# Kernel optimization log

Measured on AMD Instinct MI355X. Metric: run time of the kernel, lower is better.

The kernel has to match this reference:

```python
import jax, jax.numpy as jnp
import numpy as np

# --- HashGrid constants (from init_kwargs) ---
L = 16                 # num_lods
T = 1 << 18            # hashmap entries per level (codebook_bitwidth=18)
F = 2                  # feature_dim per level
BASE = 16              # min_width_codebook
MAXW = 1 << 12         # max_width_codebook
SCALE = np.exp((np.log(MAXW) - np.log(BASE)) / L)
RES = np.floor(BASE * SCALE ** np.arange(L)).astype(np.float32)  # per-level grid resolution
P1 = np.uint32(2654435761)  # coherent-prime hash primes (prime for x is 1)
P2 = np.uint32(805459861)
OFFS = np.array([[i, j, k] for i in (0, 1) for j in (0, 1) for k in (0, 1)], np.int32)  # [8,3] cube corners


def _hash_encode(x, tables):
    """x: [N,3] in [0,1]. tables: [L,T,F]. Returns [N, 3 + L*F] (include_xyz)."""
    def level(table, res):
        xs = x * res                              # [N,3] scaled coords
        x0 = jnp.floor(xs)
        t = xs - x0                               # fractional part
        w = t * t * (3.0 - 2.0 * t)               # Smoothstep interpolation weights
        c = x0.astype(jnp.int32)[:, None, :] + OFFS[None]    # [N,8,3] corner coords
        cu = c.astype(jnp.uint32)
        h = (cu[..., 0] ^ (cu[..., 1] * P1) ^ (cu[..., 2] * P2)) & jnp.uint32(T - 1)  # [N,8]
        feats = table[h]                          # [N,8,F] irregular gather
        wts = jnp.prod(jnp.where(OFFS[None] == 1, w[:, None, :], 1.0 - w[:, None, :]), axis=-1)  # [N,8]
        return jnp.einsum('ncf,nc->nf', feats, wts)  # [N,F]

    f = jax.vmap(level)(tables, jnp.asarray(RES))   # [L,N,F]
    f = jnp.moveaxis(f, 0, 1).reshape(x.shape[0], L * F)
    return jnp.concatenate([x, f], axis=-1)         # include_xyz prepends raw coords


def setup_inputs() -> dict:
    key = jax.random.key(0)
    k1, k2, k3, k4 = jax.random.split(key, 4)
    N = 1 << 20
    x = jax.random.uniform(k1, (N, 3), dtype=jnp.float32)
    tables = jax.random.normal(k2, (L, T, F), dtype=jnp.float32) * 1e-2
    d_in = 3 + L * F    # 35
    W1 = jax.random.normal(k3, (d_in, 128), dtype=jnp.float32) / np.sqrt(d_in)
    W2 = jax.random.normal(k4, (128, 129), dtype=jnp.float32) / np.sqrt(128.0)
    return {"x": x, "tables": tables, "W1": W1, "W2": W2}


def reference(x, tables, W1, W2):
    enc = _hash_encode(x, tables)        # [N,35]
    h = jax.nn.relu(enc @ W1)            # VanillaMLP: one hidden layer, bias-free
    return h @ W2                        # [N, 1+geo_feat_dim], Identity output act
```

## Files before the change

kernel.cpp:

```cpp
#include <hip/hip_runtime.h>

typedef __attribute__((ext_vector_type(8))) short short8;
typedef __attribute__((ext_vector_type(4))) short short4v;
typedef __attribute__((ext_vector_type(4))) float f32x4;

#define TMASK  ((1u << 18) - 1u)
#define PRIME1 2654435761u
#define PRIME2 805459861u

__constant__ float c_res[16] = {16.f, 22.f, 31.f, 45.f, 63.f, 90.f, 127.f, 181.f,
                                255.f, 362.f, 511.f, 724.f, 1023.f, 1448.f, 2047.f, 2896.f};

__device__ __forceinline__ unsigned short rne_bf16(float v) {
  unsigned u = __builtin_bit_cast(unsigned, v);
  return (unsigned short)((u + 0x7fffu + ((u >> 16) & 1u)) >> 16);
}
__device__ __forceinline__ float b2f(unsigned short h) {
  unsigned u = (unsigned)h << 16;
  return __builtin_bit_cast(float, u);
}

__global__ __launch_bounds__(256) void encode_lvl(
    const float* __restrict__ X, const float* __restrict__ Tb,
    unsigned short* __restrict__ encF) {
  const int b = blockIdx.x;
  const int g = b & 7;
  const int p = (b >> 3) * 256 + threadIdx.x;

  const float x0 = X[p * 3 + 0];
  const float x1 = X[p * 3 + 1];
  const float x2 = X[p * 3 + 2];

  short4v pk;
#pragma unroll
  for (int li = 0; li < 2; ++li) {
    const int lvl = 2 * g + li;
    const float r = c_res[lvl];
    const float xs0 = x0 * r, xs1 = x1 * r, xs2 = x2 * r;
    const float f0 = floorf(xs0), f1 = floorf(xs1), f2 = floorf(xs2);
    const float t0 = xs0 - f0, t1 = xs1 - f1, t2 = xs2 - f2;
    const float w0 = t0 * t0 * (3.f - 2.f * t0);
    const float w1v = t1 * t1 * (3.f - 2.f * t1);
    const float w2v = t2 * t2 * (3.f - 2.f * t2);
    const unsigned cx0 = (unsigned)(int)f0;
    const unsigned hy0 = (unsigned)(int)f1 * PRIME1, hy1 = hy0 + PRIME1;
    const unsigned hz0 = (unsigned)(int)f2 * PRIME2, hz1 = hz0 + PRIME2;
    const float2* tab = reinterpret_cast<const float2*>(Tb) + ((size_t)lvl << 18);
    float a0 = 0.f, a1 = 0.f;
    if (!(cx0 & 1u)) {
      const float4* tab4 = reinterpret_cast<const float4*>(tab);
#pragma unroll
      for (int jk = 0; jk < 4; ++jk) {
        const unsigned hb = (cx0 ^ ((jk & 2) ? hy1 : hy0) ^ ((jk & 1) ? hz1 : hz0)) & TMASK;
        const float4 q = tab4[hb >> 1];
        float e0x, e0y, e1x, e1y;
        if (hb & 1) { e0x = q.z; e0y = q.w; e1x = q.x; e1y = q.y; }
        else        { e0x = q.x; e0y = q.y; e1x = q.z; e1y = q.w; }
        const float wy = (jk & 2) ? w1v : 1.f - w1v;
        const float wz = (jk & 1) ? w2v : 1.f - w2v;
        const float wt0 = ((1.f - w0) * wy) * wz;
        const float wt1 = (w0 * wy) * wz;
        a0 = fmaf(e0x, wt0, a0);
        a1 = fmaf(e0y, wt0, a1);
        a0 = fmaf(e1x, wt1, a0);
        a1 = fmaf(e1y, wt1, a1);
      }
    } else {
#pragma unroll
      for (int c = 0; c < 8; ++c) {
        const unsigned hx = cx0 + (unsigned)((c >> 2) & 1);
        const unsigned hh = (hx ^ ((c & 2) ? hy1 : hy0) ^ ((c & 1) ? hz1 : hz0)) & TMASK;
        const float2 f = tab[hh];
        const float wt = (((c >> 2) & 1) ? w0 : 1.f - w0) *
                         (((c >> 1) & 1) ? w1v : 1.f - w1v) *
                         (((c & 1)) ? w2v : 1.f - w2v);
        a0 = fmaf(f.x, wt, a0);
        a1 = fmaf(f.y, wt, a1);
      }
    }
    pk[li * 2 + 0] = (short)rne_bf16(a0);
    pk[li * 2 + 1] = (short)rne_bf16(a1);
  }
  const int pl = p & 63, chunk = p >> 6;
  const size_t addr = ((size_t)(chunk * 4 + (pl >> 4)) * 64 +
                       (((g >> 1) << 4) | (pl & 15))) * 8 + (g & 1) * 4;
  *reinterpret_cast<short4v*>(encF + addr) = pk;
}

__global__ __launch_bounds__(256, 2) void mlp_mfma(
    const float* __restrict__ X, const float* __restrict__ W1,
    const float* __restrict__ W2, const unsigned short* __restrict__ encF,
    float* __restrict__ Out, int nChunks) {
  __shared__ __align__(16) unsigned char lds[76800];
  unsigned short* w1S  = (unsigned short*)lds;
  float*          w1x  = (float*)(lds + 8192);
  float*          xyzS = (float*)(lds + 9728);
  unsigned short* w2hS = (unsigned short*)(lds + 10752);
  float*          hS   = (float*)(lds + 43776);
  float*          outS = (float*)(lds + 43776);

  const int tid = threadIdx.x;
  const int lane = tid & 63, w = tid >> 6;

  for (int idx = tid; idx < 32 * 128; idx += 256) {
    const int k = idx >> 7, col = idx & 127;
    w1S[((k >> 3) * 128 + col) * 8 + (k & 7)] = rne_bf16(W1[(k + 3) * 128 + col]);
  }
  for (int idx = tid; idx < 3 * 128; idx += 256) w1x[idx] = W1[idx];
  for (int idx = tid; idx < 128 * 129; idx += 256) {
    const int k = idx / 129, col = idx - k * 129;
    w2hS[((k >> 3) * 129 + col) * 8 + (k & 7)] = rne_bf16(W2[idx]);
  }
  __syncthreads();

  const int stride = gridDim.x;
  int chunk = blockIdx.x;

  short8 af;
  float xv = 0.f;
  if (chunk < nChunks) {
    af = *reinterpret_cast<const short8*>(encF + ((size_t)(chunk * 4 + w) * 64 + lane) * 8);
    if (tid < 192) xv = X[(size_t)(chunk << 6) * 3 + tid];
  }

  for (; chunk < nChunks; chunk += stride) {
    const int row0 = chunk << 6;
    if (tid < 192) xyzS[(tid / 3) * 4 + (tid % 3)] = xv;
    __syncthreads();

    f32x4 acc1[8];
#pragma unroll
    for (int c = 0; c < 8; ++c) acc1[c] = (f32x4){0.f, 0.f, 0.f, 0.f};
#pragma unroll
    for (int c = 0; c < 8; ++c) {
      const short8 b = *reinterpret_cast<const short8*>(
          &w1S[((lane >> 4) * 128 + c * 16 + (lane & 15)) * 8]);
      acc1[c] = __builtin_amdgcn_mfma_f32_16x16x32_bf16(af, b, acc1[c], 0, 0, 0);
    }

    const int nxt = chunk + stride;
    short8 afn;
    if (nxt < nChunks) {
      afn = *reinterpret_cast<const short8*>(encF + ((size_t)(nxt * 4 + w) * 64 + lane) * 8);
      if (tid < 192) xv = X[(size_t)(nxt << 6) * 3 + tid];
    }

#pragma unroll
    for (int r = 0; r < 4; ++r) {
      const int grow = (w << 4) + (lane >> 4) * 4 + r;
      const float xs0 = xyzS[grow * 4 + 0];
      const float xs1 = xyzS[grow * 4 + 1];
      const float xs2 = xyzS[grow * 4 + 2];
#pragma unroll
      for (int c = 0; c < 8; ++c) {
        const int col = c * 16 + (lane & 15);
        float v = acc1[c][r];
        v = fmaf(xs0, w1x[col], v);
        v = fmaf(xs1, w1x[128 + col], v);
        v = fmaf(xs2, w1x[256 + col], v);
        acc1[c][r] = v;
      }
    }
#pragma unroll
    for (int c = 0; c < 8; ++c) {
#pragma unroll
      for (int r = 0; r < 4; ++r) {
        const int row = (w << 4) + (lane >> 4) * 4 + r;
        const int col = c * 16 + (lane & 15);
        const int cc = (col >> 2) ^ (row & 7);
        hS[row * 128 + (cc << 2) + (col & 3)] = fmaxf(acc1[c][r], 0.f);
      }
    }
    __syncthreads();

    {
      const int arow = (w << 4) + (lane & 15);
      short8 a2h[4], a2l[4];
#pragma unroll
      for (int kc = 0; kc < 4; ++kc) {
        const int c8 = kc * 4 + (lane >> 4);
        const int base = arow * 128;
        const int cc0 = (2 * c8) ^ (arow & 7);
        const int cc1 = (2 * c8 + 1) ^ (arow & 7);
        const f32x4 q0 = *reinterpret_cast<const f32x4*>(&hS[base + (cc0 << 2)]);
        const f32x4 q1 = *reinterpret_cast<const f32x4*>(&hS[base + (cc1 << 2)]);
#pragma unroll
        for (int e = 0; e < 4; ++e) {
          const unsigned short hi = rne_bf16(q0[e]);
          a2h[kc][e] = (short)hi;
          a2l[kc][e] = (short)rne_bf16(q0[e] - b2f(hi));
        }
#pragma unroll
        for (int e = 0; e < 4; ++e) {
          const unsigned short hi = rne_bf16(q1[e]);
          a2h[kc][4 + e] = (short)hi;
          a2l[kc][4 + e] = (short)rne_bf16(q1[e] - b2f(hi));
        }
      }
      __syncthreads();

#pragma unroll
      for (int c = 0; c < 9; ++c) {
        f32x4 acc = (f32x4){0.f, 0.f, 0.f, 0.f};
        int bcol = c * 16 + (lane & 15);
        if (bcol > 128) bcol = 128;
#pragma unroll
        for (int kc = 0; kc < 4; ++kc) {
          const int c8 = kc * 4 + (lane >> 4);
          const short8 bh = *reinterpret_cast<const short8*>(&w2hS[(c8 * 129 + bcol) * 8]);
          acc = __builtin_amdgcn_mfma_f32_16x16x32_bf16(a2h[kc], bh, acc, 0, 0, 0);
          acc = __builtin_amdgcn_mfma_f32_16x16x32_bf16(a2l[kc], bh, acc, 0, 0, 0);
        }
        const int col = c * 16 + (lane & 15);
        if (col < 129) {
#pragma unroll
          for (int r = 0; r < 4; ++r) {
            const int lrow = (w << 4) + (lane >> 4) * 4 + r;
            outS[lrow * 129 + col] = acc[r];
          }
        }
      }
    }
    __syncthreads();

    {
      float* dst = Out + (size_t)row0 * 129;
      const f32x4* src = (const f32x4*)outS;
      for (int i = tid; i < 2064; i += 256)
        *reinterpret_cast<f32x4*>(dst + 4 * i) = src[i];
    }
    af = afn;
  }
}

__global__ __launch_bounds__(256) void fused_hashmlp(
    const float* __restrict__ X, const float* __restrict__ Tb,
    const float* __restrict__ W1, const float* __restrict__ W2,
    float* __restrict__ Out, int nChunks) {
  __shared__ __align__(16) unsigned char lds[147968];
  unsigned short* w1hS = (unsigned short*)lds;
  unsigned short* w1lS = w1hS + 128 * 64;
  unsigned short* w2hS = (unsigned short*)(lds + 32768);
  unsigned short* w2lS = w2hS + 129 * 128;
  unsigned short* enchS = (unsigned short*)(lds + 98816);
  unsigned short* enclS = enchS + 64 * 64;
  float*          hS    = (float*)(lds + 115200);
  float*          outS  = (float*)(lds + 98816);

  const int tid = threadIdx.x;
  for (int idx = tid; idx < 128 * 64; idx += 256) {
    int k = idx >> 7, col = idx & 127;
    float v = 0.f;
    if (k < 35) { int r = (k < 32) ? (k + 3) : (k - 32); v = W1[r * 128 + col]; }
    unsigned short hi = rne_bf16(v);
    unsigned short lo = rne_bf16(v - b2f(hi));
    int a = col * 64 + (k ^ ((col & 7) << 3));
    w1hS[a] = hi; w1lS[a] = lo;
  }
  for (int idx = tid; idx < 129 * 128; idx += 256) {
    int k = idx / 129, col = idx - k * 129;
    float v = W2[k * 129 + col];
    unsigned short hi = rne_bf16(v);
    unsigned short lo = rne_bf16(v - b2f(hi));
    int a = col * 128 + (k ^ ((col & 7) << 3));
    w2hS[a] = hi; w2lS[a] = lo;
  }
  __syncthreads();

  const int p = tid >> 2, s = tid & 3, lane = tid & 63, w = tid >> 6;
  for (int chunk = blockIdx.x; chunk < nChunks; chunk += gridDim.x) {
    const int row0 = chunk * 64;
    {
      const int gp = row0 + p;
      const float x0 = X[gp * 3 + 0], x1 = X[gp * 3 + 1], x2 = X[gp * 3 + 2];
      short8 pkh, pkl;
#pragma unroll
      for (int li = 0; li < 4; ++li) {
        const int lvl = (s << 2) + li;
        const float r = c_res[lvl];
        const float xs0 = x0 * r, xs1 = x1 * r, xs2 = x2 * r;
        const float f0 = floorf(xs0), f1 = floorf(xs1), f2 = floorf(xs2);
        const float t0 = xs0 - f0, t1 = xs1 - f1, t2 = xs2 - f2;
        const float w0 = t0 * t0 * (3.f - 2.f * t0);
        const float w1v = t1 * t1 * (3.f - 2.f * t1);
        const float w2v = t2 * t2 * (3.f - 2.f * t2);
        const unsigned cx0 = (unsigned)(int)f0;
        const unsigned hy0 = (unsigned)(int)f1 * PRIME1, hy1 = hy0 + PRIME1;
        const unsigned hz0 = (unsigned)(int)f2 * PRIME2, hz1 = hz0 + PRIME2;
        const float2* tab = reinterpret_cast<const float2*>(Tb) + ((size_t)lvl << 18);
        float a0 = 0.f, a1 = 0.f;
#pragma unroll
        for (int c = 0; c < 8; ++c) {
          const unsigned hx = cx0 + (unsigned)((c >> 2) & 1);
          const unsigned hh = (hx ^ ((c & 2) ? hy1 : hy0) ^ ((c & 1) ? hz1 : hz0)) & TMASK;
          const float2 f = tab[hh];
          const float wt = (((c >> 2) & 1) ? w0 : 1.f - w0) *
                           (((c >> 1) & 1) ? w1v : 1.f - w1v) *
                           (((c & 1)) ? w2v : 1.f - w2v);
          a0 = fmaf(f.x, wt, a0);
          a1 = fmaf(f.y, wt, a1);
        }
        unsigned short h0 = rne_bf16(a0), h1 = rne_bf16(a1);
        pkh[li * 2 + 0] = (short)h0; pkh[li * 2 + 1] = (short)h1;
        pkl[li * 2 + 0] = (short)rne_bf16(a0 - b2f(h0));
        pkl[li * 2 + 1] = (short)rne_bf16(a1 - b2f(h1));
      }
      const int coff = (s ^ (p & 7)) << 3;
      *reinterpret_cast<short8*>(&enchS[p * 64 + coff]) = pkh;
      *reinterpret_cast<short8*>(&enclS[p * 64 + coff]) = pkl;
      short8 zh, zl;
#pragma unroll
      for (int e = 0; e < 8; ++e) { zh[e] = 0; zl[e] = 0; }
      if (s == 0) {
        unsigned short hx0 = rne_bf16(x0), hx1 = rne_bf16(x1), hx2 = rne_bf16(x2);
        zh[0] = (short)hx0; zh[1] = (short)hx1; zh[2] = (short)hx2;
        zl[0] = (short)rne_bf16(x0 - b2f(hx0));
        zl[1] = (short)rne_bf16(x1 - b2f(hx1));
        zl[2] = (short)rne_bf16(x2 - b2f(hx2));
      }
      const int coff2 = ((4 + s) ^ (p & 7)) << 3;
      *reinterpret_cast<short8*>(&enchS[p * 64 + coff2]) = zh;
      *reinterpret_cast<short8*>(&enclS[p * 64 + coff2]) = zl;
    }
    __syncthreads();
    f32x4 acc1[8];
#pragma unroll
    for (int c = 0; c < 8; ++c) acc1[c] = (f32x4){0.f, 0.f, 0.f, 0.f};
    {
      const int arow = (w << 4) + (lane & 15);
#pragma unroll
      for (int kc = 0; kc < 2; ++kc) {
        const int c8 = kc * 4 + (lane >> 4);
        const int aoff = arow * 64 + ((c8 ^ (arow & 7)) << 3);
        const short8 ah = *reinterpret_cast<const short8*>(&enchS[aoff]);
        const short8 al = *reinterpret_cast<const short8*>(&enclS[aoff]);
#pragma unroll
        for (int c = 0; c < 8; ++c) {
          const int bcol = c * 16 + (lane & 15);
          const int boff = bcol * 64 + ((c8 ^ (bcol & 7)) << 3);
          const short8 bh = *reinterpret_cast<const short8*>(&w1hS[boff]);
          const short8 bl = *reinterpret_cast<const short8*>(&w1lS[boff]);
          acc1[c] = __builtin_amdgcn_mfma_f32_16x16x32_bf16(ah, bh, acc1[c], 0, 0, 0);
          acc1[c] = __builtin_amdgcn_mfma_f32_16x16x32_bf16(ah, bl, acc1[c], 0, 0, 0);
          acc1[c] = __builtin_amdgcn_mfma_f32_16x16x32_bf16(al, bh, acc1[c], 0, 0, 0);
        }
      }
    }
#pragma unroll
    for (int c = 0; c < 8; ++c) {
#pragma unroll
      for (int r = 0; r < 4; ++r) {
        const int row = (w << 4) + (lane >> 4) * 4 + r;
        const int col = c * 16 + (lane & 15);
        const int cc = (col >> 2) ^ (row & 7);
        hS[row * 128 + (cc << 2) + (col & 3)] = fmaxf(acc1[c][r], 0.f);
      }
    }
    __syncthreads();
    {
      const int arow = (w << 4) + (lane & 15);
      short8 a2h[4], a2l[4];
#pragma unroll
      for (int kc = 0; kc < 4; ++kc) {
        const int c8 = kc * 4 + (lane >> 4);
        const int base = arow * 128;
        const int cc0 = (2 * c8) ^ (arow & 7);
        const int cc1 = (2 * c8 + 1) ^ (arow & 7);
        const f32x4 q0 = *reinterpret_cast<const f32x4*>(&hS[base + (cc0 << 2)]);
        const f32x4 q1 = *reinterpret_cast<const f32x4*>(&hS[base + (cc1 << 2)]);
#pragma unroll
        for (int e = 0; e < 4; ++e) {
          unsigned short hi = rne_bf16(q0[e]);
          a2h[kc][e] = (short)hi;
          a2l[kc][e] = (short)rne_bf16(q0[e] - b2f(hi));
        }
#pragma unroll
        for (int e = 0; e < 4; ++e) {
          unsigned short hi = rne_bf16(q1[e]);
          a2h[kc][4 + e] = (short)hi;
          a2l[kc][4 + e] = (short)rne_bf16(q1[e] - b2f(hi));
        }
      }
      __syncthreads();
#pragma unroll
      for (int c = 0; c < 9; ++c) {
        f32x4 acc = (f32x4){0.f, 0.f, 0.f, 0.f};
        int bcol = c * 16 + (lane & 15);
        if (bcol > 128) bcol = 128;
#pragma unroll
        for (int kc = 0; kc < 4; ++kc) {
          const int c8 = kc * 4 + (lane >> 4);
          const int boff = bcol * 128 + ((c8 ^ (bcol & 7)) << 3);
          const short8 bh = *reinterpret_cast<const short8*>(&w2hS[boff]);
          const short8 bl = *reinterpret_cast<const short8*>(&w2lS[boff]);
          acc = __builtin_amdgcn_mfma_f32_16x16x32_bf16(a2h[kc], bh, acc, 0, 0, 0);
          acc = __builtin_amdgcn_mfma_f32_16x16x32_bf16(a2h[kc], bl, acc, 0, 0, 0);
          acc = __builtin_amdgcn_mfma_f32_16x16x32_bf16(a2l[kc], bh, acc, 0, 0, 0);
        }
        const int col = c * 16 + (lane & 15);
        if (col < 129) {
#pragma unroll
          for (int r = 0; r < 4; ++r) {
            const int lrow = (w << 4) + (lane >> 4) * 4 + r;
            outS[lrow * 129 + col] = acc[r];
          }
        }
      }
    }
    __syncthreads();
    {
      float* dst = Out + (size_t)row0 * 129;
      const f32x4* src = (const f32x4*)outS;
      for (int i = tid; i < 2064; i += 256)
        *reinterpret_cast<f32x4*>(dst + 4 * i) = src[i];
    }
    __syncthreads();
  }
}

extern "C" void kernel_launch(void* const* d_in, const int* in_sizes, int n_in,
                              void* d_out, int out_size, void* d_ws, size_t ws_size,
                              hipStream_t stream) {
  const float* X  = (const float*)d_in[0];
  const float* Tb = (const float*)d_in[1];
  const float* W1 = (const float*)d_in[2];
  const float* W2 = (const float*)d_in[3];
  float* Out = (float*)d_out;

  const int N = in_sizes[0] / 3;
  const int nChunks = N / 64;

  const size_t encBytes = (size_t)nChunks * 4096;
  if (ws_size >= encBytes && (N & 255) == 0) {
    unsigned short* encF = (unsigned short*)d_ws;
    encode_lvl<<<(N / 256) * 8, 256, 0, stream>>>(X, Tb, encF);
    mlp_mfma<<<2048, 256, 0, stream>>>(X, W1, W2, encF, Out, nChunks);
  } else {
    int grid = nChunks < 1024 ? nChunks : 1024;
    fused_hashmlp<<<grid, 256, 0, stream>>>(X, Tb, W1, W2, Out, nChunks);
  }
}
```

Measured before the change: 577.9 us.

## Fuse encode and MLP into one persistent kernel with flag-based producer-consumer sync

Replaces the separate encode and MLP kernels with one persistent kernel of 512 blocks. Each block encodes a level pair (g, 15-g) for groups of 256 points and signals completion through per-group atomic counters. Blocks then run the MFMA MLP on chunks whose counters reach 8, spinning with s_sleep when none are ready. This overlaps gather-bound encoding with compute-bound MLP work and removes the second launch. The cost is atomics, system-scope loads, a memset, and a specialization to N = 2^20. The design also depends on all 512 blocks being co-resident to avoid deadlock, and it drops the prefetch of the next chunk.

```diff
diff --git a/kernel.cpp b/kernel.cpp
--- a/kernel.cpp
+++ b/kernel.cpp
@@ -1,8 +1,8 @@
 #include <hip/hip_runtime.h>
 
 typedef __attribute__((ext_vector_type(8))) short short8;
-typedef __attribute__((ext_vector_type(4))) short short4v;
 typedef __attribute__((ext_vector_type(4))) float f32x4;
+typedef __attribute__((ext_vector_type(4))) int int4v;
 
 #define TMASK  ((1u << 18) - 1u)
 #define PRIME1 2654435761u
@@ -20,78 +20,59 @@
   return __builtin_bit_cast(float, u);
 }
 
-__global__ __launch_bounds__(256) void encode_lvl(
+__device__ __forceinline__ float2 enc_level(float x0, float x1, float x2, int lvl,
+                                            const float* __restrict__ Tb) {
+  const float r = c_res[lvl];
+  const float xs0 = x0 * r, xs1 = x1 * r, xs2 = x2 * r;
+  const float f0 = floorf(xs0), f1 = floorf(xs1), f2 = floorf(xs2);
+  const float t0 = xs0 - f0, t1 = xs1 - f1, t2 = xs2 - f2;
+  const float w0 = t0 * t0 * (3.f - 2.f * t0);
+  const float w1v = t1 * t1 * (3.f - 2.f * t1);
+  const float w2v = t2 * t2 * (3.f - 2.f * t2);
+  const unsigned cx0 = (unsigned)(int)f0;
+  const unsigned hy0 = (unsigned)(int)f1 * PRIME1, hy1 = hy0 + PRIME1;
+  const unsigned hz0 = (unsigned)(int)f2 * PRIME2, hz1 = hz0 + PRIME2;
+  const float2* tab = reinterpret_cast<const float2*>(Tb) + ((size_t)lvl << 18);
+  float a0 = 0.f, a1 = 0.f;
+  if (!(cx0 & 1u)) {
+    const float4* tab4 = reinterpret_cast<const float4*>(tab);
+#pragma unroll
+    for (int jk = 0; jk < 4; ++jk) {
+      const unsigned hb = (cx0 ^ ((jk & 2) ? hy1 : hy0) ^ ((jk & 1) ? hz1 : hz0)) & TMASK;
+      const float4 q = tab4[hb >> 1];
+      float e0x, e0y, e1x, e1y;
+      if (hb & 1) { e0x = q.z; e0y = q.w; e1x = q.x; e1y = q.y; }
+      else        { e0x = q.x; e0y = q.y; e1x = q.z; e1y = q.w; }
+      const float wy = (jk & 2) ? w1v : 1.f - w1v;
+      const float wz = (jk & 1) ? w2v : 1.f - w2v;
+      const float wt0 = ((1.f - w0) * wy) * wz;
+      const float wt1 = (w0 * wy) * wz;
+      a0 = fmaf(e0x, wt0, a0); a1 = fmaf(e0y, wt0, a1);
+      a0 = fmaf(e1x, wt1, a0); a1 = fmaf(e1y, wt1, a1);
+    }
+  } else {
+#pragma unroll
+    for (int c = 0; c < 8; ++c) {
+      const unsigned hx = cx0 + (unsigned)((c >> 2) & 1);
+      const unsigned hh = (hx ^ ((c & 2) ? hy1 : hy0) ^ ((c & 1) ? hz1 : hz0)) & TMASK;
+      const float2 f = tab[hh];
+      const float wt = (((c >> 2) & 1) ? w0 : 1.f - w0) *
+                       (((c >> 1) & 1) ? w1v : 1.f - w1v) *
+                       (((c & 1)) ? w2v : 1.f - w2v);
+      a0 = fmaf(f.x, wt, a0);
+      a1 = fmaf(f.y, wt, a1);
+    }
+  }
+  return make_float2(a0, a1);
+}
+
+__global__ __launch_bounds__(256, 2) void fused_pc(
     const float* __restrict__ X, const float* __restrict__ Tb,
-    unsigned short* __restrict__ encF) {
-  const int b = blockIdx.x;
-  const int g = b & 7;
-  const int p = (b >> 3) * 256 + threadIdx.x;
-
-  const float x0 = X[p * 3 + 0];
-  const float x1 = X[p * 3 + 1];
-  const float x2 = X[p * 3 + 2];
-
-  short4v pk;
-#pragma unroll
-  for (int li = 0; li < 2; ++li) {
-    const int lvl = 2 * g + li;
-    const float r = c_res[lvl];
-    const float xs0 = x0 * r, xs1 = x1 * r, xs2 = x2 * r;
-    const float f0 = floorf(xs0), f1 = floorf(xs1), f2 = floorf(xs2);
-    const float t0 = xs0 - f0, t1 = xs1 - f1, t2 = xs2 - f2;
-    const float w0 = t0 * t0 * (3.f - 2.f * t0);
-    const float w1v = t1 * t1 * (3.f - 2.f * t1);
-    const float w2v = t2 * t2 * (3.f - 2.f * t2);
-    const unsigned cx0 = (unsigned)(int)f0;
-    const unsigned hy0 = (unsigned)(int)f1 * PRIME1, hy1 = hy0 + PRIME1;
-    const unsigned hz0 = (unsigned)(int)f2 * PRIME2, hz1 = hz0 + PRIME2;
-    const float2* tab = reinterpret_cast<const float2*>(Tb) + ((size_t)lvl << 18);
-    float a0 = 0.f, a1 = 0.f;
-    if (!(cx0 & 1u)) {
-      const float4* tab4 = reinterpret_cast<const float4*>(tab);
-#pragma unroll
-      for (int jk = 0; jk < 4; ++jk) {
-        const unsigned hb = (cx0 ^ ((jk & 2) ? hy1 : hy0) ^ ((jk & 1) ? hz1 : hz0)) & TMASK;
-        const float4 q = tab4[hb >> 1];
-        float e0x, e0y, e1x, e1y;
-        if (hb & 1) { e0x = q.z; e0y = q.w; e1x = q.x; e1y = q.y; }
-        else        { e0x = q.x; e0y = q.y; e1x = q.z; e1y = q.w; }
-        const float wy = (jk & 2) ? w1v : 1.f - w1v;
-        const float wz = (jk & 1) ? w2v : 1.f - w2v;
-        const float wt0 = ((1.f - w0) * wy) * wz;
-        const float wt1 = (w0 * wy) * wz;
-        a0 = fmaf(e0x, wt0, a0);
-        a1 = fmaf(e0y, wt0, a1);
-        a0 = fmaf(e1x, wt1, a0);
-        a1 = fmaf(e1y, wt1, a1);
-      }
-    } else {
-#pragma unroll
-      for (int c = 0; c < 8; ++c) {
-        const unsigned hx = cx0 + (unsigned)((c >> 2) & 1);
-        const unsigned hh = (hx ^ ((c & 2) ? hy1 : hy0) ^ ((c & 1) ? hz1 : hz0)) & TMASK;
-        const float2 f = tab[hh];
-        const float wt = (((c >> 2) & 1) ? w0 : 1.f - w0) *
-                         (((c >> 1) & 1) ? w1v : 1.f - w1v) *
-                         (((c & 1)) ? w2v : 1.f - w2v);
-        a0 = fmaf(f.x, wt, a0);
-        a1 = fmaf(f.y, wt, a1);
-      }
-    }
-    pk[li * 2 + 0] = (short)rne_bf16(a0);
-    pk[li * 2 + 1] = (short)rne_bf16(a1);
-  }
-  const int pl = p & 63, chunk = p >> 6;
-  const size_t addr = ((size_t)(chunk * 4 + (pl >> 4)) * 64 +
-                       (((g >> 1) << 4) | (pl & 15))) * 8 + (g & 1) * 4;
-  *reinterpret_cast<short4v*>(encF + addr) = pk;
-}
-
-__global__ __launch_bounds__(256, 2) void mlp_mfma(
-    const float* __restrict__ X, const float* __restrict__ W1,
-    const float* __restrict__ W2, const unsigned short* __restrict__ encF,
-    float* __restrict__ Out, int nChunks) {
+    const float* __restrict__ W1, const float* __restrict__ W2,
+    unsigned short* __restrict__ encF, int* __restrict__ flags,
+    float* __restrict__ Out) {
   __shared__ __align__(16) unsigned char lds[76800];
+  __shared__ int ldsflag;
   unsigned short* w1S  = (unsigned short*)lds;
   float*          w1x  = (float*)(lds + 8192);
   float*          xyzS = (float*)(lds + 9728);
@@ -101,6 +82,10 @@
 
   const int tid = threadIdx.x;
   const int lane = tid & 63, w = tid >> 6;
+  const int b = blockIdx.x;
+  const int g = b & 7;
+  const int bslot = b >> 3;
+  const int lvlA = g, lvlB = 15 - g;
 
   for (int idx = tid; idx < 32 * 128; idx += 256) {
     const int k = idx >> 7, col = idx & 127;
@@ -113,19 +98,18 @@
   }
   __syncthreads();
 
-  const int stride = gridDim.x;
-  int chunk = blockIdx.x;
-
-  short8 af;
-  float xv = 0.f;
-  if (chunk < nChunks) {
-    af = *reinterpret_cast<const short8*>(encF + ((size_t)(chunk * 4 + w) * 64 + lane) * 8);
-    if (tid < 192) xv = X[(size_t)(chunk << 6) * 3 + tid];
-  }
-
-  for (; chunk < nChunks; chunk += stride) {
+  int nextI = 0;
+
+  auto mlp_chunk = [&](int chunk) {
+    const size_t base_int = ((size_t)(chunk * 4 + w) * 64 + lane) * 4;
+    int4v ai;
+#pragma unroll
+    for (int e = 0; e < 4; ++e)
+      ai[e] = __hip_atomic_load((int*)encF + base_int + e,
+                                __ATOMIC_RELAXED, __HIP_MEMORY_SCOPE_SYSTEM);
+    const short8 af = __builtin_bit_cast(short8, ai);
     const int row0 = chunk << 6;
-    if (tid < 192) xyzS[(tid / 3) * 4 + (tid % 3)] = xv;
+    if (tid < 192) xyzS[(tid / 3) * 4 + (tid % 3)] = X[(size_t)row0 * 3 + tid];
     __syncthreads();
 
     f32x4 acc1[8];
@@ -133,18 +117,10 @@
     for (int c = 0; c < 8; ++c) acc1[c] = (f32x4){0.f, 0.f, 0.f, 0.f};
 #pragma unroll
     for (int c = 0; c < 8; ++c) {
-      const short8 b = *reinterpret_cast<const short8*>(
+      const short8 bb = *reinterpret_cast<const short8*>(
           &w1S[((lane >> 4) * 128 + c * 16 + (lane & 15)) * 8]);
-      acc1[c] = __builtin_amdgcn_mfma_f32_16x16x32_bf16(af, b, acc1[c], 0, 0, 0);
-    }
-
-    const int nxt = chunk + stride;
-    short8 afn;
-    if (nxt < nChunks) {
-      afn = *reinterpret_cast<const short8*>(encF + ((size_t)(nxt * 4 + w) * 64 + lane) * 8);
-      if (tid < 192) xv = X[(size_t)(nxt << 6) * 3 + tid];
-    }
-
+      acc1[c] = __builtin_amdgcn_mfma_f32_16x16x32_bf16(af, bb, acc1[c], 0, 0, 0);
+    }
 #pragma unroll
     for (int r = 0; r < 4; ++r) {
       const int grow = (w << 4) + (lane >> 4) * 4 + r;
@@ -173,63 +149,109 @@
     }
     __syncthreads();
 
-    {
-      const int arow = (w << 4) + (lane & 15);
-      short8 a2h[4], a2l[4];
+    const int arow = (w << 4) + (lane & 15);
+    short8 a2h[4], a2l[4];
+#pragma unroll
+    for (int kc = 0; kc < 4; ++kc) {
+      const int c8 = kc * 4 + (lane >> 4);
+      const int base = arow * 128;
+      const int cc0 = (2 * c8) ^ (arow & 7);
+      const int cc1 = (2 * c8 + 1) ^ (arow & 7);
+      const f32x4 q0 = *reinterpret_cast<const f32x4*>(&hS[base + (cc0 << 2)]);
+      const f32x4 q1 = *reinterpret_cast<const f32x4*>(&hS[base + (cc1 << 2)]);
+#pragma unroll
+      for (int e = 0; e < 4; ++e) {
+        const unsigned short hi = rne_bf16(q0[e]);
+        a2h[kc][e] = (short)hi;
+        a2l[kc][e] = (short)rne_bf16(q0[e] - b2f(hi));
+      }
+#pragma unroll
+      for (int e = 0; e < 4; ++e) {
+        const unsigned short hi = rne_bf16(q1[e]);
+        a2h[kc][4 + e] = (short)hi;
+        a2l[kc][4 + e] = (short)rne_bf16(q1[e] - b2f(hi));
+      }
+    }
+    __syncthreads();
+
+#pragma unroll
+    for (int c = 0; c < 9; ++c) {
+      f32x4 acc = (f32x4){0.f, 0.f, 0.f, 0.f};
+      int bcol = c * 16 + (lane & 15);
+      if (bcol > 128) bcol = 128;
 #pragma unroll
       for (int kc = 0; kc < 4; ++kc) {
         const int c8 = kc * 4 + (lane >> 4);
-        const int base = arow * 128;
-        const int cc0 = (2 * c8) ^ (arow & 7);
-        const int cc1 = (2 * c8 + 1) ^ (arow & 7);
-        const f32x4 q0 = *reinterpret_cast<const f32x4*>(&hS[base + (cc0 << 2)]);
-        const f32x4 q1 = *reinterpret_cast<const f32x4*>(&hS[base + (cc1 << 2)]);
-#pragma unroll
-        for (int e = 0; e < 4; ++e) {
-          const unsigned short hi = rne_bf16(q0[e]);
-          a2h[kc][e] = (short)hi;
-          a2l[kc][e] = (short)rne_bf16(q0[e] - b2f(hi));
-        }
-#pragma unroll
-        for (int e = 0; e < 4; ++e) {
-          const unsigned short hi = rne_bf16(q1[e]);
-          a2h[kc][4 + e] = (short)hi;
-          a2l[kc][4 + e] = (short)rne_bf16(q1[e] - b2f(hi));
-        }
-      }
+        const short8 bh = *reinterpret_cast<const short8*>(&w2hS[(c8 * 129 + bcol) * 8]);
+        acc = __builtin_amdgcn_mfma_f32_16x16x32_bf16(a2h[kc], bh, acc, 0, 0, 0);
+        acc = __builtin_amdgcn_mfma_f32_16x16x32_bf16(a2l[kc], bh, acc, 0, 0, 0);
+      }
+      const int col = c * 16 + (lane & 15);
+      if (col < 129) {
+#pragma unroll
+        for (int r = 0; r < 4; ++r) {
+          const int lrow = (w << 4) + (lane >> 4) * 4 + r;
+          outS[lrow * 129 + col] = acc[r];
+        }
+      }
+    }
+    __syncthreads();
+
+    float* dst = Out + (size_t)row0 * 129;
+    const f32x4* src = (const f32x4*)outS;
+    for (int i = tid; i < 2064; i += 256)
+      __builtin_nontemporal_store(src[i], reinterpret_cast<f32x4*>(dst + 4 * i));
+  };
+
+  for (int t = 0; t < 64; ++t) {
+    const int grp = bslot + t * 64;
+    {
+      const int p = (grp << 8) + tid;
+      const float x0 = X[p * 3 + 0];
+      const float x1 = X[p * 3 + 1];
+      const float x2 = X[p * 3 + 2];
+      const int pl = p & 63, chunk = p >> 6;
+      const size_t rowbase = ((size_t)(chunk * 4 + (pl >> 4)) * 64 + (pl & 15)) * 8;
+#pragma unroll
+      for (int li = 0; li < 2; ++li) {
+        const int lvl = li ? lvlB : lvlA;
+        const float2 a = enc_level(x0, x1, x2, lvl, Tb);
+        const int c8 = lvl >> 2;
+        const size_t addr_short = rowbase + (size_t)(c8 << 7) + (lvl & 3) * 2;
+        const int val = (int)rne_bf16(a.x) | ((int)rne_bf16(a.y) << 16);
+        __hip_atomic_store((int*)encF + (addr_short >> 1), val,
+                           __ATOMIC_RELAXED, __HIP_MEMORY_SCOPE_SYSTEM);
+      }
+    }
+    __syncthreads();
+    if (tid == 0)
+      __hip_atomic_fetch_add(&flags[grp], 1, __ATOMIC_RELAXED, __HIP_MEMORY_SCOPE_SYSTEM);
+
+    while (nextI < 32) {
+      const int c = b + (nextI << 9);
+      if (tid == 0)
+        ldsflag = __hip_atomic_load(&flags[c >> 2], __ATOMIC_RELAXED,
+                                    __HIP_MEMORY_SCOPE_SYSTEM);
       __syncthreads();
-
-#pragma unroll
-      for (int c = 0; c < 9; ++c) {
-        f32x4 acc = (f32x4){0.f, 0.f, 0.f, 0.f};
-        int bcol = c * 16 + (lane & 15);
-        if (bcol > 128) bcol = 128;
-#pragma unroll
-        for (int kc = 0; kc < 4; ++kc) {
-          const int c8 = kc * 4 + (lane >> 4);
-          const short8 bh = *reinterpret_cast<const short8*>(&w2hS[(c8 * 129 + bcol) * 8]);
-          acc = __builtin_amdgcn_mfma_f32_16x16x32_bf16(a2h[kc], bh, acc, 0, 0, 0);
-          acc = __builtin_amdgcn_mfma_f32_16x16x32_bf16(a2l[kc], bh, acc, 0, 0, 0);
-        }
-        const int col = c * 16 + (lane & 15);
-        if (col < 129) {
-#pragma unroll
-          for (int r = 0; r < 4; ++r) {
-            const int lrow = (w << 4) + (lane >> 4) * 4 + r;
-            outS[lrow * 129 + col] = acc[r];
-          }
-        }
-      }
-    }
-    __syncthreads();
-
-    {
-      float* dst = Out + (size_t)row0 * 129;
-      const f32x4* src = (const f32x4*)outS;
-      for (int i = tid; i < 2064; i += 256)
-        *reinterpret_cast<f32x4*>(dst + 4 * i) = src[i];
-    }
-    af = afn;
+      if (ldsflag != 8) break;
+      mlp_chunk(c);
+      ++nextI;
+    }
+  }
+
+  while (nextI < 32) {
+    const int c = b + (nextI << 9);
+    for (;;) {
+      if (tid == 0)
+        ldsflag = __hip_atomic_load(&flags[c >> 2], __ATOMIC_RELAXED,
+                                    __HIP_MEMORY_SCOPE_SYSTEM);
+      __syncthreads();
+      if (ldsflag == 8) break;
+      __builtin_amdgcn_s_sleep(32);
+      __syncthreads();
+    }
+    mlp_chunk(c);
+    ++nextI;
   }
 }
 
@@ -277,33 +299,11 @@
 #pragma unroll
       for (int li = 0; li < 4; ++li) {
         const int lvl = (s << 2) + li;
-        const float r = c_res[lvl];
-        const float xs0 = x0 * r, xs1 = x1 * r, xs2 = x2 * r;
-        const float f0 = floorf(xs0), f1 = floorf(xs1), f2 = floorf(xs2);
-        const float t0 = xs0 - f0, t1 = xs1 - f1, t2 = xs2 - f2;
-        const float w0 = t0 * t0 * (3.f - 2.f * t0);
-        const float w1v = t1 * t1 * (3.f - 2.f * t1);
-        const float w2v = t2 * t2 * (3.f - 2.f * t2);
-        const unsigned cx0 = (unsigned)(int)f0;
-        const unsigned hy0 = (unsigned)(int)f1 * PRIME1, hy1 = hy0 + PRIME1;
-        const unsigned hz0 = (unsigned)(int)f2 * PRIME2, hz1 = hz0 + PRIME2;
-        const float2* tab = reinterpret_cast<const float2*>(Tb) + ((size_t)lvl << 18);
-        float a0 = 0.f, a1 = 0.f;
-#pragma unroll
-        for (int c = 0; c < 8; ++c) {
-          const unsigned hx = cx0 + (unsigned)((c >> 2) & 1);
-          const unsigned hh = (hx ^ ((c & 2) ? hy1 : hy0) ^ ((c & 1) ? hz1 : hz0)) & TMASK;
-          const float2 f = tab[hh];
-          const float wt = (((c >> 2) & 1) ? w0 : 1.f - w0) *
-                           (((c >> 1) & 1) ? w1v : 1.f - w1v) *
-                           (((c & 1)) ? w2v : 1.f - w2v);
-          a0 = fmaf(f.x, wt, a0);
-          a1 = fmaf(f.y, wt, a1);
-        }
-        unsigned short h0 = rne_bf16(a0), h1 = rne_bf16(a1);
+        const float2 a = enc_level(x0, x1, x2, lvl, Tb);
+        unsigned short h0 = rne_bf16(a.x), h1 = rne_bf16(a.y);
         pkh[li * 2 + 0] = (short)h0; pkh[li * 2 + 1] = (short)h1;
-        pkl[li * 2 + 0] = (short)rne_bf16(a0 - b2f(h0));
-        pkl[li * 2 + 1] = (short)rne_bf16(a1 - b2f(h1));
+        pkl[li * 2 + 0] = (short)rne_bf16(a.x - b2f(h0));
+        pkl[li * 2 + 1] = (short)rne_bf16(a.y - b2f(h1));
       }
       const int coff = (s ^ (p & 7)) << 3;
       *reinterpret_cast<short8*>(&enchS[p * 64 + coff]) = pkh;
@@ -431,10 +431,12 @@
   const int nChunks = N / 64;
 
   const size_t encBytes = (size_t)nChunks * 4096;
-  if (ws_size >= encBytes && (N & 255) == 0) {
+  const size_t flagBytes = 4096 * sizeof(int);
+  if (N == (1 << 20) && ws_size >= encBytes + flagBytes) {
     unsigned short* encF = (unsigned short*)d_ws;
-    encode_lvl<<<(N / 256) * 8, 256, 0, stream>>>(X, Tb, encF);
-    mlp_mfma<<<2048, 256, 0, stream>>>(X, W1, W2, encF, Out, nChunks);
+    int* flags = (int*)((char*)d_ws + encBytes);
+    hipMemsetAsync(flags, 0, flagBytes, stream);
+    fused_pc<<<512, 256, 0, stream>>>(X, Tb, W1, W2, encF, flags, Out);
   } else {
     int grid = nChunks < 1024 ? nChunks : 1024;
     fused_hashmlp<<<grid, 256, 0, stream>>>(X, Tb, W1, W2, Out, nChunks);
```

Result: slower. 642.6 us (+11.2%).

## Move W2 bf16 fragments to global, shrink LDS, keep xyz in registers

Applied to the files above, without the earlier changes.

A small prep kernel now converts W2 to bf16 in the per-lane MFMA fragment layout and writes it to workspace. The MLP kernel then streams these fragments from global memory (expected to hit L2) instead of staging W2 in LDS, which cuts LDS use from about 75KB to about 42KB and allows occupancy 3. The xyz rows are loaded straight into registers, which removes the xyzS LDS staging and one barrier. Output stores become nontemporal, and the grid shrinks to 768 persistent blocks. The trade-off is that W2 reads now travel through global memory or cache rather than LDS, and an extra barrier is added at the end of each chunk.

```diff
diff --git a/kernel.cpp b/kernel.cpp
--- a/kernel.cpp
+++ b/kernel.cpp
@@ -60,10 +60,8 @@
         const float wz = (jk & 1) ? w2v : 1.f - w2v;
         const float wt0 = ((1.f - w0) * wy) * wz;
         const float wt1 = (w0 * wy) * wz;
-        a0 = fmaf(e0x, wt0, a0);
-        a1 = fmaf(e0y, wt0, a1);
-        a0 = fmaf(e1x, wt1, a0);
-        a1 = fmaf(e1y, wt1, a1);
+        a0 = fmaf(e0x, wt0, a0); a1 = fmaf(e0y, wt0, a1);
+        a0 = fmaf(e1x, wt1, a0); a1 = fmaf(e1y, wt1, a1);
       }
     } else {
 #pragma unroll
@@ -87,17 +85,29 @@
   *reinterpret_cast<short4v*>(encF + addr) = pk;
 }
 
-__global__ __launch_bounds__(256, 2) void mlp_mfma(
+__global__ __launch_bounds__(64) void prep_w2hi(
+    const float* __restrict__ W2, unsigned short* __restrict__ w2hi) {
+  const int lane = threadIdx.x;
+  const int c = blockIdx.x >> 2, kc = blockIdx.x & 3;
+  int bcol = c * 16 + (lane & 15);
+  if (bcol > 128) bcol = 128;
+  const int k0 = (kc * 4 + (lane >> 4)) * 8;
+  short8 v;
+#pragma unroll
+  for (int e = 0; e < 8; ++e)
+    v[e] = (short)rne_bf16(W2[(size_t)(k0 + e) * 129 + bcol]);
+  *reinterpret_cast<short8*>(w2hi + ((size_t)blockIdx.x * 64 + lane) * 8) = v;
+}
+
+__global__ __launch_bounds__(256, 3) void mlp_mfma(
     const float* __restrict__ X, const float* __restrict__ W1,
-    const float* __restrict__ W2, const unsigned short* __restrict__ encF,
+    const unsigned short* __restrict__ encF, const unsigned short* __restrict__ w2hi,
     float* __restrict__ Out, int nChunks) {
-  __shared__ __align__(16) unsigned char lds[76800];
-  unsigned short* w1S  = (unsigned short*)lds;
-  float*          w1x  = (float*)(lds + 8192);
-  float*          xyzS = (float*)(lds + 9728);
-  unsigned short* w2hS = (unsigned short*)(lds + 10752);
-  float*          hS   = (float*)(lds + 43776);
-  float*          outS = (float*)(lds + 43776);
+  __shared__ __align__(16) unsigned char lds[42752];
+  unsigned short* w1S = (unsigned short*)lds;
+  float*          w1x = (float*)(lds + 8192);
+  float*          hS  = (float*)(lds + 9728);
+  float*          outS = (float*)(lds + 9728);
 
   const int tid = threadIdx.x;
   const int lane = tid & 63, w = tid >> 6;
@@ -107,57 +117,56 @@
     w1S[((k >> 3) * 128 + col) * 8 + (k & 7)] = rne_bf16(W1[(k + 3) * 128 + col]);
   }
   for (int idx = tid; idx < 3 * 128; idx += 256) w1x[idx] = W1[idx];
-  for (int idx = tid; idx < 128 * 129; idx += 256) {
-    const int k = idx / 129, col = idx - k * 129;
-    w2hS[((k >> 3) * 129 + col) * 8 + (k & 7)] = rne_bf16(W2[idx]);
-  }
   __syncthreads();
 
   const int stride = gridDim.x;
   int chunk = blockIdx.x;
 
   short8 af;
-  float xv = 0.f;
+  float xr0[4], xr1[4], xr2[4];
   if (chunk < nChunks) {
     af = *reinterpret_cast<const short8*>(encF + ((size_t)(chunk * 4 + w) * 64 + lane) * 8);
-    if (tid < 192) xv = X[(size_t)(chunk << 6) * 3 + tid];
+#pragma unroll
+    for (int r = 0; r < 4; ++r) {
+      const size_t row = (size_t)(chunk << 6) + (w << 4) + (lane >> 4) * 4 + r;
+      xr0[r] = X[row * 3 + 0]; xr1[r] = X[row * 3 + 1]; xr2[r] = X[row * 3 + 2];
+    }
   }
 
   for (; chunk < nChunks; chunk += stride) {
     const int row0 = chunk << 6;
-    if (tid < 192) xyzS[(tid / 3) * 4 + (tid % 3)] = xv;
-    __syncthreads();
 
     f32x4 acc1[8];
 #pragma unroll
     for (int c = 0; c < 8; ++c) acc1[c] = (f32x4){0.f, 0.f, 0.f, 0.f};
 #pragma unroll
     for (int c = 0; c < 8; ++c) {
-      const short8 b = *reinterpret_cast<const short8*>(
+      const short8 bb = *reinterpret_cast<const short8*>(
           &w1S[((lane >> 4) * 128 + c * 16 + (lane & 15)) * 8]);
-      acc1[c] = __builtin_amdgcn_mfma_f32_16x16x32_bf16(af, b, acc1[c], 0, 0, 0);
+      acc1[c] = __builtin_amdgcn_mfma_f32_16x16x32_bf16(af, bb, acc1[c], 0, 0, 0);
     }
 
     const int nxt = chunk + stride;
     short8 afn;
+    float xn0[4], xn1[4], xn2[4];
     if (nxt < nChunks) {
       afn = *reinterpret_cast<const short8*>(encF + ((size_t)(nxt * 4 + w) * 64 + lane) * 8);
-      if (tid < 192) xv = X[(size_t)(nxt << 6) * 3 + tid];
+#pragma unroll
+      for (int r = 0; r < 4; ++r) {
+        const size_t row = (size_t)(nxt << 6) + (w << 4) + (lane >> 4) * 4 + r;
+        xn0[r] = X[row * 3 + 0]; xn1[r] = X[row * 3 + 1]; xn2[r] = X[row * 3 + 2];
+      }
     }
 
 #pragma unroll
     for (int r = 0; r < 4; ++r) {
-      const int grow = (w << 4) + (lane >> 4) * 4 + r;
-      const float xs0 = xyzS[grow * 4 + 0];
-      const float xs1 = xyzS[grow * 4 + 1];
-      const float xs2 = xyzS[grow * 4 + 2];
 #pragma unroll
       for (int c = 0; c < 8; ++c) {
         const int col = c * 16 + (lane & 15);
         float v = acc1[c][r];
-        v = fmaf(xs0, w1x[col], v);
-        v = fmaf(xs1, w1x[128 + col], v);
-        v = fmaf(xs2, w1x[256 + col], v);
+        v = fmaf(xr0[r], w1x[col], v);
+        v = fmaf(xr1[r], w1x[128 + col], v);
+        v = fmaf(xr2[r], w1x[256 + col], v);
         acc1[c][r] = v;
       }
     }
@@ -202,12 +211,10 @@
 #pragma unroll
       for (int c = 0; c < 9; ++c) {
         f32x4 acc = (f32x4){0.f, 0.f, 0.f, 0.f};
-        int bcol = c * 16 + (lane & 15);
-        if (bcol > 128) bcol = 128;
 #pragma unroll
         for (int kc = 0; kc < 4; ++kc) {
-          const int c8 = kc * 4 + (lane >> 4);
-          const short8 bh = *reinterpret_cast<const short8*>(&w2hS[(c8 * 129 + bcol) * 8]);
+          const short8 bh = *reinterpret_cast<const short8*>(
+              w2hi + ((size_t)((c * 4 + kc) * 64 + lane)) * 8);
           acc = __builtin_amdgcn_mfma_f32_16x16x32_bf16(a2h[kc], bh, acc, 0, 0, 0);
           acc = __builtin_amdgcn_mfma_f32_16x16x32_bf16(a2l[kc], bh, acc, 0, 0, 0);
         }
@@ -227,9 +234,12 @@
       float* dst = Out + (size_t)row0 * 129;
       const f32x4* src = (const f32x4*)outS;
       for (int i = tid; i < 2064; i += 256)
-        *reinterpret_cast<f32x4*>(dst + 4 * i) = src[i];
-    }
+        __builtin_nontemporal_store(src[i], reinterpret_cast<f32x4*>(dst + 4 * i));
+    }
+    __syncthreads();
     af = afn;
+#pragma unroll
+    for (int r = 0; r < 4; ++r) { xr0[r] = xn0[r]; xr1[r] = xn1[r]; xr2[r] = xn2[r]; }
   }
 }
 
@@ -431,10 +441,13 @@
   const int nChunks = N / 64;
 
   const size_t encBytes = (size_t)nChunks * 4096;
-  if (ws_size >= encBytes && (N & 255) == 0) {
+  const size_t w2hiBytes = 36 * 64 * 16;
+  if (ws_size >= encBytes + w2hiBytes && (N & 255) == 0) {
     unsigned short* encF = (unsigned short*)d_ws;
+    unsigned short* w2hi = (unsigned short*)((char*)d_ws + encBytes);
     encode_lvl<<<(N / 256) * 8, 256, 0, stream>>>(X, Tb, encF);
-    mlp_mfma<<<2048, 256, 0, stream>>>(X, W1, W2, encF, Out, nChunks);
+    prep_w2hi<<<36, 64, 0, stream>>>(W2, w2hi);
+    mlp_mfma<<<768, 256, 0, stream>>>(X, W1, encF, w2hi, Out, nChunks);
   } else {
     int grid = nChunks < 1024 ? nChunks : 1024;
     fused_hashmlp<<<grid, 256, 0, stream>>>(X, Tb, W1, W2, Out, nChunks);
```

New measurement: 794.9 us. 1.38x slower.
